# Performance work log

Measured on AMD Instinct MI355X. Metric: run time of the kernel, lower is better.

Reference implementation:

```python
import jax, jax.numpy as jnp
import numpy as np
from jax import lax

B, CIN, L = 2048, 1024, 30
E, C = 8, 2            # num_experts, num_classes
FC_IN = 256 * 9        # 2304
FIN_IN = C + 512 * L + 256 * (L // 2 + 1)  # 19458


def _maxpool1d(x):
    # MaxPool1d(kernel=2, stride=2, padding=1); pad with -inf like torch
    return lax.reduce_window(x, -jnp.inf, lax.max,
                             (1, 1, 2), (1, 1, 2),
                             [(0, 0), (0, 0), (1, 1)])


def _conv1d(x, w):
    # x: [B,Cin,L], w: [Cout,Cin,3], padding=1
    return lax.conv_general_dilated(x, w, (1,), [(1, 1)],
                                    dimension_numbers=('NCH', 'OIH', 'NCH'))


def setup_inputs() -> dict:
    key = jax.random.key(0)
    ks = jax.random.split(key, 16)
    s = 0.02
    inp = {
        'x': jax.random.normal(ks[0], (B, CIN, L), jnp.float32),
        'expert_idx': jax.random.randint(ks[1], (B,), 0, E),
        'conv1_w': jax.random.normal(ks[2], (512, 1024, 3), jnp.float32) * s,
        'conv1_b': jnp.zeros((512,), jnp.float32),
        'conv2_w': jax.random.normal(ks[3], (256, 512, 3), jnp.float32) * s,
        'conv2_b': jnp.zeros((256,), jnp.float32),
        'fc_w': jax.random.normal(ks[4], (1024, FC_IN), jnp.float32) * s,
        'fc_b': jnp.zeros((1024,), jnp.float32),
        'e_w1': jax.random.normal(ks[5], (E, 512, 1024), jnp.float32) * s,
        'e_b1': jnp.zeros((E, 512), jnp.float32),
        'e_w2': jax.random.normal(ks[6], (E, C, 512), jnp.float32) * s,
        'e_b2': jnp.zeros((E, C), jnp.float32),
        'agg_w': jax.random.normal(ks[7], (C, E * C), jnp.float32) * s,
        'agg_b': jnp.zeros((C,), jnp.float32),
        'fin_w': jax.random.normal(ks[8], (C, FIN_IN), jnp.float32) * s,
        'fin_b': jnp.zeros((C,), jnp.float32),
    }
    return inp


def reference(x, expert_idx, conv1_w, conv1_b, conv2_w, conv2_b, fc_w, fc_b,
              e_w1, e_b1, e_w2, e_b2, agg_w, agg_b, fin_w, fin_b):
    b = x.shape[0]
    # shared feature extractor
    x1 = jax.nn.relu(_conv1d(x, conv1_w) + conv1_b[None, :, None])     # [B,512,30]
    p1 = _maxpool1d(x1)                                                 # [B,512,16]
    x2 = jax.nn.relu(_conv1d(p1, conv2_w) + conv2_b[None, :, None])    # [B,256,16]
    p2 = _maxpool1d(x2)                                                 # [B,256,9]
    sf = jax.nn.relu(p2.reshape(b, -1) @ fc_w.T + fc_b)                 # [B,1024]

    # expert dispatch: run all experts densely, then select per-sample
    h = jax.nn.relu(jnp.einsum('bd,ehd->beh', sf, e_w1) + e_b1)        # [B,E,512]
    all_out = jnp.einsum('beh,ech->bec', h, e_w2) + e_b2               # [B,E,C]
    sel = all_out[jnp.arange(b), expert_idx]                           # [B,C]
    oh = jax.nn.one_hot(expert_idx, E, dtype=sel.dtype)                # [B,E]
    expert_outputs = (oh[:, :, None] * sel[:, None, :]).reshape(b, E * C)

    agg = expert_outputs @ agg_w.T + agg_b                             # [B,C]
    combined = jnp.concatenate(
        [agg, x1.reshape(b, -1), x2.reshape(b, -1)], axis=1)           # [B,19458]
    return combined @ fin_w.T + fin_b                                  # [B,C]
```

## Files before the change

kernel.cpp:

```cpp
#include <hip/hip_runtime.h>
#include <hip/hip_bf16.h>

typedef short short8 __attribute__((ext_vector_type(8)));
typedef short short4v __attribute__((ext_vector_type(4)));
typedef float f32x4 __attribute__((ext_vector_type(4)));

__device__ __forceinline__ float bf2f(short s) {
  return __builtin_bit_cast(float, (unsigned)((unsigned short)s) << 16);
}
__device__ __forceinline__ short f2bf(float f) {
  return __builtin_bit_cast(short, __float2bfloat16(f));
}
__device__ __forceinline__ void g2lds16(const void* g, void* l) {
  __builtin_amdgcn_global_load_lds((const __attribute__((address_space(1))) void*)g,
                                   (__attribute__((address_space(3))) void*)l, 16, 0, 0);
}


__global__ __launch_bounds__(256) void prep_x(const float* __restrict__ x, short* __restrict__ xt) {
  __shared__ float tile[64 * 30];
  const int b = blockIdx.x, ci0 = blockIdx.y * 64, t = threadIdx.x;
  const float* src = x + ((long)b * 1024 + ci0) * 30;
  for (int i = t; i < 1920; i += 256) tile[i] = src[i];
  __syncthreads();
  short* dst = xt + (long)b * 32 * 1024 + ci0;
  for (int i = t; i < 2048; i += 256) {
    int lp = i >> 6, ci = i & 63;
    float v = (lp == 0 || lp == 31) ? 0.f : tile[ci * 30 + lp - 1];
    dst[(long)lp * 1024 + ci] = f2bf(v);
  }
}

__global__ __launch_bounds__(256) void prep_weights(
    const float* __restrict__ conv1_w, const float* __restrict__ conv2_w,
    const float* __restrict__ fc_w, const float* __restrict__ e_w1,
    const float* __restrict__ fin_w,
    short* __restrict__ w1t, short* __restrict__ w2t, short* __restrict__ fcwt,
    short* __restrict__ ew1t, float* __restrict__ finw1, float* __restrict__ finw2) {
  const int T0 = 1572864;
  const int T1 = T0 + 393216;
  const int T2 = T1 + 2359296;
  const int T3 = T2 + 4194304;
  const int T4 = T3 + 30720;
  const int T5 = T4 + 8192;
  for (long idx = (long)blockIdx.x * 256 + threadIdx.x; idx < T5;
       idx += (long)gridDim.x * 256) {
    if (idx < T0) {
      int i = (int)idx; int co = i / 3072, j = i % 3072, k = j >> 10, ci = j & 1023;
      w1t[i] = f2bf(conv1_w[(co * 1024 + ci) * 3 + k]);
    } else if (idx < T1) {
      int i = (int)(idx - T0); int co = i / 1536, j = i % 1536, k = j >> 9, ci = j & 511;
      w2t[i] = f2bf(conv2_w[(co * 512 + ci) * 3 + k]);
    } else if (idx < T2) {
      int i = (int)(idx - T1); int n = i / 2304, j = i % 2304, jj = j >> 8, co = j & 255;
      fcwt[i] = f2bf(fc_w[n * 2304 + co * 9 + jj]);
    } else if (idx < T3) {
      int i = (int)(idx - T2);
      ew1t[i] = f2bf(e_w1[i]);
    } else if (idx < T4) {
      int i = (int)(idx - T3); int c = i / 15360, r = i % 15360, l = r >> 9, co = r & 511;
      finw1[i] = fin_w[c * 19458 + 2 + co * 30 + l];
    } else {
      int i = (int)(idx - T4); int c = i / 4096, r = i % 4096, l = r >> 8, co = r & 255;
      finw2[i] = fin_w[c * 19458 + 2 + 15360 + co * 16 + l];
    }
  }
}

__global__ __launch_bounds__(512, 2) void gemm256_bt_relu(
    const short* __restrict__ A, const short* __restrict__ Bm, short* __restrict__ C,
    const float* __restrict__ bias, int N, int K, int L, int S1, int S2, int nNB) {
  __shared__ __align__(16) short lA0[256 * 64], lA1[256 * 64];
  __shared__ __align__(16) short lB0[256 * 64], lB1[256 * 64];
  const int t = threadIdx.x, wave = t >> 6, lane = t & 63;
  const int wr = wave >> 2, wc = wave & 3;
  const int nwg = gridDim.x, qn = nwg >> 3, bid = blockIdx.x;
  const int swz = (bid & 7) * qn + (bid >> 3);
  const int m0 = (swz / nNB) * 256, n0 = (swz % nNB) * 256;
  const int srow = t >> 3;
  const int scol = ((t & 7) ^ (srow & 7)) * 8;

  long aoff[4], boff[4];
#pragma unroll
  for (int q = 0; q < 4; ++q) {
    int m = m0 + q * 64 + srow;
    aoff[q] = (long)(m / L) * S1 + (long)(m % L) * S2 + scol;
    boff[q] = (long)(n0 + q * 64 + srow) * K + scol;
  }
  const int ldst = wave * 512 + lane * 8;

  f32x4 acc[8][4];
#pragma unroll
  for (int i = 0; i < 8; ++i)
#pragma unroll
    for (int j = 0; j < 4; ++j) acc[i][j] = f32x4{0.f, 0.f, 0.f, 0.f};

  const int l7 = lane & 7, g4 = lane >> 4, r16 = lane & 15;
  const int nK = K >> 6;

#define STAGE256(k0, dA, dB) do {                                     \
    const long kk0_ = (long)(k0);                                     \
    _Pragma("unroll")                                                 \
    for (int q = 0; q < 4; ++q) {                                     \
      g2lds16(A + aoff[q] + kk0_, &dA[q * 4096 + ldst]);              \
      g2lds16(Bm + boff[q] + kk0_, &dB[q * 4096 + ldst]);             \
    } } while (0)

#define PHASES256(sA, sB) do {                                                        \
    short8 af[4][2], bfr[4][2];                                                       \
                                 \
    _Pragma("unroll") for (int kk = 0; kk < 2; ++kk) {                                \
      const int jb = ((kk * 4 + g4) ^ l7) * 8;                                        \
      _Pragma("unroll") for (int i = 0; i < 4; ++i)                                   \
        af[i][kk] = *(const short8*)&sA[(wr * 128 + i * 16 + r16) * 64 + jb];         \
      _Pragma("unroll") for (int j = 0; j < 2; ++j)                                   \
        bfr[j][kk] = *(const short8*)&sB[(wc * 64 + j * 16 + r16) * 64 + jb];         \
    }                                                                                 \
    __builtin_amdgcn_s_setprio(1);                                                    \
    _Pragma("unroll") for (int i = 0; i < 4; ++i)                                     \
    _Pragma("unroll") for (int j = 0; j < 2; ++j)                                     \
    _Pragma("unroll") for (int kk = 0; kk < 2; ++kk)                                  \
      acc[i][j] = __builtin_amdgcn_mfma_f32_16x16x32_bf16(af[i][kk], bfr[j][kk], acc[i][j], 0, 0, 0); \
    __builtin_amdgcn_s_setprio(0);                                                    \
                                         \
    _Pragma("unroll") for (int kk = 0; kk < 2; ++kk) {                                \
      const int jb = ((kk * 4 + g4) ^ l7) * 8;                                        \
      _Pragma("unroll") for (int j = 0; j < 2; ++j)                                   \
        bfr[2 + j][kk] = *(const short8*)&sB[(wc * 64 + (2 + j) * 16 + r16) * 64 + jb]; \
    }                                                                                 \
    __builtin_amdgcn_s_setprio(1);                                                    \
    _Pragma("unroll") for (int i = 0; i < 4; ++i)                                     \
    _Pragma("unroll") for (int j = 0; j < 2; ++j)                                     \
    _Pragma("unroll") for (int kk = 0; kk < 2; ++kk)                                  \
      acc[i][2 + j] = __builtin_amdgcn_mfma_f32_16x16x32_bf16(af[i][kk], bfr[2 + j][kk], acc[i][2 + j], 0, 0, 0); \
    __builtin_amdgcn_s_setprio(0);                                                    \
                                         \
    _Pragma("unroll") for (int kk = 0; kk < 2; ++kk) {                                \
      const int jb = ((kk * 4 + g4) ^ l7) * 8;                                        \
      _Pragma("unroll") for (int i = 0; i < 4; ++i)                                   \
        af[i][kk] = *(const short8*)&sA[(wr * 128 + (4 + i) * 16 + r16) * 64 + jb];   \
    }                                                                                 \
    __builtin_amdgcn_s_setprio(1);                                                    \
    _Pragma("unroll") for (int i = 0; i < 4; ++i)                                     \
    _Pragma("unroll") for (int j = 0; j < 2; ++j)                                     \
    _Pragma("unroll") for (int kk = 0; kk < 2; ++kk)                                  \
      acc[4 + i][2 + j] = __builtin_amdgcn_mfma_f32_16x16x32_bf16(af[i][kk], bfr[2 + j][kk], acc[4 + i][2 + j], 0, 0, 0); \
    __builtin_amdgcn_s_setprio(0);                                                    \
                                \
    __builtin_amdgcn_s_setprio(1);                                                    \
    _Pragma("unroll") for (int i = 0; i < 4; ++i)                                     \
    _Pragma("unroll") for (int j = 0; j < 2; ++j)                                     \
    _Pragma("unroll") for (int kk = 0; kk < 2; ++kk)                                  \
      acc[4 + i][j] = __builtin_amdgcn_mfma_f32_16x16x32_bf16(af[i][kk], bfr[j][kk], acc[4 + i][j], 0, 0, 0); \
    __builtin_amdgcn_s_setprio(0);                                                    \
  } while (0)

  STAGE256(0, lA0, lB0);
  for (int ktp = 0; ktp < (nK >> 1); ++ktp) {
    const int t1 = 2 * ktp + 1;
    __syncthreads();
    STAGE256((long)t1 << 6, lA1, lB1);
    PHASES256(lA0, lB0);
    __syncthreads();
    if (t1 + 1 < nK) STAGE256((long)(t1 + 1) << 6, lA0, lB0);
    PHASES256(lA1, lB1);
  }

#pragma unroll
  for (int j = 0; j < 4; ++j) {
    int col = n0 + wc * 64 + j * 16 + r16;
    float bv = bias[col];
#pragma unroll
    for (int i = 0; i < 8; ++i) {
      int rbase = m0 + wr * 128 + i * 16 + (g4 << 2);
#pragma unroll
      for (int r = 0; r < 4; ++r) {
        float o = fmaxf(acc[i][j][r] + bv, 0.f);
        C[(long)(rbase + r) * N + col] = f2bf(o);
      }
    }
  }
#undef STAGE256
#undef PHASES256
}

__global__ __launch_bounds__(256) void gemm_bt_relu(
    const short* __restrict__ A, const short* __restrict__ Bm, short* __restrict__ C,
    const float* __restrict__ bias, int N, int K, int L, int S1, int S2, int nNB) {
  __shared__ __align__(16) short lA[128 * 64];
  __shared__ __align__(16) short lB[128 * 64];
  const int t = threadIdx.x, wave = t >> 6, lane = t & 63;
  const int wr = wave >> 1, wc = wave & 1;
  const int nwg = gridDim.x, q = nwg >> 3, bid = blockIdx.x;
  const int swz = (bid & 7) * q + (bid >> 3);
  const int m0 = (swz / nNB) * 128, n0 = (swz % nNB) * 128;
  const int arow = t >> 3;
  const int sw8 = arow & 7;
  const int acolg = (((t & 7) ^ sw8) * 8);

  long aoff[4], boff[4];
#pragma unroll
  for (int qq = 0; qq < 4; ++qq) {
    int m = m0 + qq * 32 + arow;
    aoff[qq] = (long)(m / L) * S1 + (long)(m % L) * S2 + acolg;
    boff[qq] = (long)(n0 + qq * 32 + arow) * K + acolg;
  }

  f32x4 acc[4][4];
#pragma unroll
  for (int i = 0; i < 4; ++i)
#pragma unroll
    for (int j = 0; j < 4; ++j) acc[i][j] = f32x4{0.f, 0.f, 0.f, 0.f};

  const int l7 = lane & 7, g4 = lane >> 4, r16 = lane & 15;
  const int nK = K >> 6;
  for (int kt = 0; kt < nK; ++kt) {
    const int k0 = kt << 6;
#pragma unroll
    for (int qq = 0; qq < 4; ++qq) {
      g2lds16(A + aoff[qq] + k0, &lA[qq * 2048 + wave * 512 + lane * 8]);
      g2lds16(Bm + boff[qq] + k0, &lB[qq * 2048 + wave * 512 + lane * 8]);
    }
    __syncthreads();
#pragma unroll
    for (int kk = 0; kk < 2; ++kk) {
      const int jblk = ((kk * 4 + g4) ^ l7) * 8;
      short8 af[4], bfv[4];
#pragma unroll
      for (int i = 0; i < 4; ++i)
        af[i] = *(const short8*)&lA[(wr * 64 + i * 16 + r16) * 64 + jblk];
#pragma unroll
      for (int j = 0; j < 4; ++j)
        bfv[j] = *(const short8*)&lB[(wc * 64 + j * 16 + r16) * 64 + jblk];
#pragma unroll
      for (int i = 0; i < 4; ++i)
#pragma unroll
        for (int j = 0; j < 4; ++j)
          acc[i][j] = __builtin_amdgcn_mfma_f32_16x16x32_bf16(af[i], bfv[j], acc[i][j], 0, 0, 0);
    }
    __syncthreads();
  }

#pragma unroll
  for (int j = 0; j < 4; ++j) {
    int col = n0 + wc * 64 + j * 16 + (lane & 15);
    float bv = bias[col];
#pragma unroll
    for (int i = 0; i < 4; ++i) {
      int rbase = m0 + wr * 64 + i * 16 + ((lane >> 4) << 2);
#pragma unroll
      for (int r = 0; r < 4; ++r) {
        float o = fmaxf(acc[i][j][r] + bv, 0.f);
        C[(long)(rbase + r) * N + col] = f2bf(o);
      }
    }
  }
}

__global__ __launch_bounds__(256) void pool1(const short* __restrict__ x1t, short* __restrict__ p1t) {
  const long total = (long)2048 * 18 * 128;
  for (long idx = (long)blockIdx.x * 256 + threadIdx.x; idx < total;
       idx += (long)gridDim.x * 256) {
    int c4 = (int)(idx & 127); long tmp = idx >> 7; int jp = (int)(tmp % 18); long b = tmp / 18;
    short4v v = {0, 0, 0, 0};
    if (jp >= 1 && jp <= 16) {
      int j = jp - 1;
      int l0 = 2 * j - 1, l1 = 2 * j;
      short4v a = (l0 >= 0) ? *(const short4v*)&x1t[(b * 30 + l0) * 512 + c4 * 4] : short4v{0, 0, 0, 0};
      short4v bb = (l1 < 30) ? *(const short4v*)&x1t[(b * 30 + l1) * 512 + c4 * 4] : short4v{0, 0, 0, 0};
#pragma unroll
      for (int u = 0; u < 4; ++u) v[u] = f2bf(fmaxf(bf2f(a[u]), bf2f(bb[u])));
    }
    *(short4v*)&p1t[idx * 4] = v;
  }
}

__global__ __launch_bounds__(256) void pool2(const short* __restrict__ x2t, short* __restrict__ p2t) {
  const long total = (long)2048 * 9 * 64;
  for (long idx = (long)blockIdx.x * 256 + threadIdx.x; idx < total;
       idx += (long)gridDim.x * 256) {
    int c4 = (int)(idx & 63); long tmp = idx >> 6; int j = (int)(tmp % 9); long b = tmp / 9;
    int l0 = 2 * j - 1, l1 = 2 * j;
    short4v a = (l0 >= 0) ? *(const short4v*)&x2t[(b * 16 + l0) * 256 + c4 * 4] : short4v{0, 0, 0, 0};
    short4v bb = (l1 < 16) ? *(const short4v*)&x2t[(b * 16 + l1) * 256 + c4 * 4] : short4v{0, 0, 0, 0};
    short4v v;
#pragma unroll
    for (int u = 0; u < 4; ++u) v[u] = f2bf(fmaxf(bf2f(a[u]), bf2f(bb[u])));
    *(short4v*)&p2t[idx * 4] = v;
  }
}

__global__ __launch_bounds__(256) void final_k(
    const short* __restrict__ h, const short* __restrict__ x1t, const short* __restrict__ x2t,
    const int* __restrict__ eidx, const float* __restrict__ e_w2, const float* __restrict__ e_b2,
    const float* __restrict__ agg_w, const float* __restrict__ agg_b,
    const float* __restrict__ fin_w, const float* __restrict__ fin_b,
    const float* __restrict__ finw1, const float* __restrict__ finw2,
    float* __restrict__ out) {
  const int b = blockIdx.x, t = threadIdx.x, lane = t & 63, wave = t >> 6;
  const int e = eidx[b];
  float s0 = 0.f, s1 = 0.f, f0 = 0.f, f1 = 0.f;
  {
    const short* hp = h + (long)b * 4096 + e * 512;
    const float* w20 = e_w2 + (e * 2 + 0) * 512;
    const float* w21 = e_w2 + (e * 2 + 1) * 512;
    for (int i = t; i < 512; i += 256) {
      float hv = bf2f(hp[i]);
      s0 += hv * w20[i];
      s1 += hv * w21[i];
    }
  }
  {
    const short* xp = x1t + (long)b * 15360;
#pragma unroll
    for (int it = 0; it < 15; ++it) {
      int i = (it * 256 + t) * 4;
      short4v xv = *(const short4v*)&xp[i];
      float4 w0 = *(const float4*)&finw1[i];
      float4 w1 = *(const float4*)&finw1[15360 + i];
      float a0 = bf2f(xv[0]), a1 = bf2f(xv[1]), a2 = bf2f(xv[2]), a3 = bf2f(xv[3]);
      f0 += a0 * w0.x + a1 * w0.y + a2 * w0.z + a3 * w0.w;
      f1 += a0 * w1.x + a1 * w1.y + a2 * w1.z + a3 * w1.w;
    }
    const short* x2p = x2t + (long)b * 4096;
#pragma unroll
    for (int it = 0; it < 4; ++it) {
      int i = (it * 256 + t) * 4;
      short4v xv = *(const short4v*)&x2p[i];
      float4 w0 = *(const float4*)&finw2[i];
      float4 w1 = *(const float4*)&finw2[4096 + i];
      float a0 = bf2f(xv[0]), a1 = bf2f(xv[1]), a2 = bf2f(xv[2]), a3 = bf2f(xv[3]);
      f0 += a0 * w0.x + a1 * w0.y + a2 * w0.z + a3 * w0.w;
      f1 += a0 * w1.x + a1 * w1.y + a2 * w1.z + a3 * w1.w;
    }
  }
#pragma unroll
  for (int off = 32; off > 0; off >>= 1) {
    s0 += __shfl_down(s0, off);
    s1 += __shfl_down(s1, off);
    f0 += __shfl_down(f0, off);
    f1 += __shfl_down(f1, off);
  }
  __shared__ float red[4][4];
  if (lane == 0) { red[wave][0] = s0; red[wave][1] = s1; red[wave][2] = f0; red[wave][3] = f1; }
  __syncthreads();
  if (t == 0) {
    float S0 = 0, S1 = 0, F0 = 0, F1 = 0;
    for (int w = 0; w < 4; ++w) { S0 += red[w][0]; S1 += red[w][1]; F0 += red[w][2]; F1 += red[w][3]; }
    float sel0 = S0 + e_b2[e * 2 + 0];
    float sel1 = S1 + e_b2[e * 2 + 1];
    float agg0 = sel0 * agg_w[e * 2] + sel1 * agg_w[e * 2 + 1] + agg_b[0];
    float agg1 = sel0 * agg_w[16 + e * 2] + sel1 * agg_w[16 + e * 2 + 1] + agg_b[1];
    out[b * 2 + 0] = F0 + agg0 * fin_w[0] + agg1 * fin_w[1] + fin_b[0];
    out[b * 2 + 1] = F1 + agg0 * fin_w[19458 + 0] + agg1 * fin_w[19458 + 1] + fin_b[1];
  }
}

extern "C" void kernel_launch(void* const* d_in, const int* in_sizes, int n_in,
                              void* d_out, int out_size, void* d_ws, size_t ws_size,
                              hipStream_t stream) {
  const float* x       = (const float*)d_in[0];
  const int*   eidx    = (const int*)d_in[1];
  const float* conv1_w = (const float*)d_in[2];
  const float* conv1_b = (const float*)d_in[3];
  const float* conv2_w = (const float*)d_in[4];
  const float* conv2_b = (const float*)d_in[5];
  const float* fc_w    = (const float*)d_in[6];
  const float* fc_b    = (const float*)d_in[7];
  const float* e_w1    = (const float*)d_in[8];
  const float* e_b1    = (const float*)d_in[9];
  const float* e_w2    = (const float*)d_in[10];
  const float* e_b2    = (const float*)d_in[11];
  const float* agg_w   = (const float*)d_in[12];
  const float* agg_b   = (const float*)d_in[13];
  const float* fin_w   = (const float*)d_in[14];
  const float* fin_b   = (const float*)d_in[15];
  float* out = (float*)d_out;

  char* ws = (char*)d_ws;
  short* xt    = (short*)(ws + 0L);
  short* x1t   = (short*)(ws + 134217728L);
  short* p1t   = (short*)(ws + 197132288L);
  short* x2t   = (short*)(ws + 234881024L);
  short* p2t   = (short*)(ws + 251658240L);
  short* sf    = (short*)(ws + 261095424L);
  short* h     = (short*)(ws + 265289728L);
  short* w1t   = (short*)(ws + 282066944L);
  short* w2t   = (short*)(ws + 285212672L);
  short* fcwt  = (short*)(ws + 285999104L);
  short* ew1t  = (short*)(ws + 290717696L);
  float* finw1 = (float*)(ws + 299106304L);
  float* finw2 = (float*)(ws + 299229184L);

  prep_weights<<<4096, 256, 0, stream>>>(conv1_w, conv2_w, fc_w, e_w1, fin_w,
                                         w1t, w2t, fcwt, ew1t, finw1, finw2);
  prep_x<<<dim3(2048, 16), 256, 0, stream>>>(x, xt);
  gemm256_bt_relu<<<480, 512, 0, stream>>>(xt, w1t, x1t, conv1_b, 512, 3072, 30, 32768, 1024, 2);
  pool1<<<2048, 256, 0, stream>>>(x1t, p1t);
  gemm_bt_relu<<<512, 256, 0, stream>>>(p1t, w2t, x2t, conv2_b, 256, 1536, 16, 9216, 512, 2);
  pool2<<<1024, 256, 0, stream>>>(x2t, p2t);
  gemm_bt_relu<<<128, 256, 0, stream>>>(p2t, fcwt, sf, fc_b, 1024, 2304, 1, 2304, 0, 8);
  gemm_bt_relu<<<512, 256, 0, stream>>>(sf, ew1t, h, e_b1, 4096, 1024, 1, 1024, 0, 32);
  final_k<<<2048, 256, 0, stream>>>(h, x1t, x2t, eidx, e_w2, e_b2, agg_w, agg_b,
                                    fin_w, fin_b, finw1, finw2, out);
}
```

Before: 445.1 us.

## Double-buffer LDS in 128-tile GEMM and vectorize input transpose

Converts the 128x128 GEMM used for conv2, fc and expert layer 1 to double-buffered LDS. The next K tile is prefetched while MFMAs run on the current one, with s_setprio raised around the MFMA block. This removes one barrier-bound load stall per K step but doubles LDS use per block. The input transpose kernel also switches to float4 loads and 4-wide bf16 stores, cutting memory instruction count.

```diff
diff --git a/kernel.cpp b/kernel.cpp
--- a/kernel.cpp
+++ b/kernel.cpp
@@ -21,13 +21,18 @@
   __shared__ float tile[64 * 30];
   const int b = blockIdx.x, ci0 = blockIdx.y * 64, t = threadIdx.x;
   const float* src = x + ((long)b * 1024 + ci0) * 30;
-  for (int i = t; i < 1920; i += 256) tile[i] = src[i];
+  for (int i = t; i < 480; i += 256)
+    ((float4*)tile)[i] = ((const float4*)src)[i];
   __syncthreads();
   short* dst = xt + (long)b * 32 * 1024 + ci0;
-  for (int i = t; i < 2048; i += 256) {
-    int lp = i >> 6, ci = i & 63;
-    float v = (lp == 0 || lp == 31) ? 0.f : tile[ci * 30 + lp - 1];
-    dst[(long)lp * 1024 + ci] = f2bf(v);
+  for (int i = t; i < 512; i += 256) {
+    int lp = i >> 4, cq = i & 15;
+    short4v v = {0, 0, 0, 0};
+    if (lp >= 1 && lp <= 30) {
+#pragma unroll
+      for (int u = 0; u < 4; ++u) v[u] = f2bf(tile[(cq * 4 + u) * 30 + lp - 1]);
+    }
+    *(short4v*)&dst[(long)lp * 1024 + cq * 4] = v;
   }
 }
 
@@ -78,7 +83,7 @@
   const int swz = (bid & 7) * qn + (bid >> 3);
   const int m0 = (swz / nNB) * 256, n0 = (swz % nNB) * 256;
   const int srow = t >> 3;
-  const int scol = ((t & 7) ^ (srow & 7)) * 8;
+  const int scol = (((t & 7) ^ (srow & 7)) * 8);
 
   long aoff[4], boff[4];
 #pragma unroll
@@ -184,19 +189,18 @@
 #undef PHASES256
 }
 
-__global__ __launch_bounds__(256) void gemm_bt_relu(
+__global__ __launch_bounds__(256, 2) void gemm128_bt_relu(
     const short* __restrict__ A, const short* __restrict__ Bm, short* __restrict__ C,
     const float* __restrict__ bias, int N, int K, int L, int S1, int S2, int nNB) {
-  __shared__ __align__(16) short lA[128 * 64];
-  __shared__ __align__(16) short lB[128 * 64];
+  __shared__ __align__(16) short lA0[128 * 64], lA1[128 * 64];
+  __shared__ __align__(16) short lB0[128 * 64], lB1[128 * 64];
   const int t = threadIdx.x, wave = t >> 6, lane = t & 63;
   const int wr = wave >> 1, wc = wave & 1;
-  const int nwg = gridDim.x, q = nwg >> 3, bid = blockIdx.x;
-  const int swz = (bid & 7) * q + (bid >> 3);
+  const int nwg = gridDim.x, qn = nwg >> 3, bid = blockIdx.x;
+  const int swz = (bid & 7) * qn + (bid >> 3);
   const int m0 = (swz / nNB) * 128, n0 = (swz % nNB) * 128;
   const int arow = t >> 3;
-  const int sw8 = arow & 7;
-  const int acolg = (((t & 7) ^ sw8) * 8);
+  const int acolg = (((t & 7) ^ (arow & 7)) * 8);
 
   long aoff[4], boff[4];
 #pragma unroll
@@ -205,6 +209,7 @@
     aoff[qq] = (long)(m / L) * S1 + (long)(m % L) * S2 + acolg;
     boff[qq] = (long)(n0 + qq * 32 + arow) * K + acolg;
   }
+  const int ldst = wave * 512 + lane * 8;
 
   f32x4 acc[4][4];
 #pragma unroll
@@ -214,40 +219,49 @@
 
   const int l7 = lane & 7, g4 = lane >> 4, r16 = lane & 15;
   const int nK = K >> 6;
-  for (int kt = 0; kt < nK; ++kt) {
-    const int k0 = kt << 6;
-#pragma unroll
-    for (int qq = 0; qq < 4; ++qq) {
-      g2lds16(A + aoff[qq] + k0, &lA[qq * 2048 + wave * 512 + lane * 8]);
-      g2lds16(Bm + boff[qq] + k0, &lB[qq * 2048 + wave * 512 + lane * 8]);
-    }
+
+#define STAGE128(k0, dA, dB) do {                                     \
+    const long kk0_ = (long)(k0);                                     \
+    _Pragma("unroll")                                                 \
+    for (int qq = 0; qq < 4; ++qq) {                                  \
+      g2lds16(A + aoff[qq] + kk0_, &dA[qq * 2048 + ldst]);            \
+      g2lds16(Bm + boff[qq] + kk0_, &dB[qq * 2048 + ldst]);           \
+    } } while (0)
+
+#define PHASES128(sA, sB) do {                                                        \
+    _Pragma("unroll")                                                                 \
+    for (int kk = 0; kk < 2; ++kk) {                                                  \
+      const int jblk = ((kk * 4 + g4) ^ l7) * 8;                                      \
+      short8 af[4], bfv[4];                                                           \
+      _Pragma("unroll") for (int i = 0; i < 4; ++i)                                   \
+        af[i] = *(const short8*)&sA[(wr * 64 + i * 16 + r16) * 64 + jblk];            \
+      _Pragma("unroll") for (int j = 0; j < 4; ++j)                                   \
+        bfv[j] = *(const short8*)&sB[(wc * 64 + j * 16 + r16) * 64 + jblk];           \
+      __builtin_amdgcn_s_setprio(1);                                                  \
+      _Pragma("unroll") for (int i = 0; i < 4; ++i)                                   \
+      _Pragma("unroll") for (int j = 0; j < 4; ++j)                                   \
+        acc[i][j] = __builtin_amdgcn_mfma_f32_16x16x32_bf16(af[i], bfv[j], acc[i][j], 0, 0, 0); \
+      __builtin_amdgcn_s_setprio(0);                                                  \
+    } } while (0)
+
+  STAGE128(0, lA0, lB0);
+  for (int ktp = 0; ktp < (nK >> 1); ++ktp) {
+    const int t1 = 2 * ktp + 1;
     __syncthreads();
-#pragma unroll
-    for (int kk = 0; kk < 2; ++kk) {
-      const int jblk = ((kk * 4 + g4) ^ l7) * 8;
-      short8 af[4], bfv[4];
-#pragma unroll
-      for (int i = 0; i < 4; ++i)
-        af[i] = *(const short8*)&lA[(wr * 64 + i * 16 + r16) * 64 + jblk];
-#pragma unroll
-      for (int j = 0; j < 4; ++j)
-        bfv[j] = *(const short8*)&lB[(wc * 64 + j * 16 + r16) * 64 + jblk];
-#pragma unroll
-      for (int i = 0; i < 4; ++i)
-#pragma unroll
-        for (int j = 0; j < 4; ++j)
-          acc[i][j] = __builtin_amdgcn_mfma_f32_16x16x32_bf16(af[i], bfv[j], acc[i][j], 0, 0, 0);
-    }
+    STAGE128((long)t1 << 6, lA1, lB1);
+    PHASES128(lA0, lB0);
     __syncthreads();
+    if (t1 + 1 < nK) STAGE128((long)(t1 + 1) << 6, lA0, lB0);
+    PHASES128(lA1, lB1);
   }
 
 #pragma unroll
   for (int j = 0; j < 4; ++j) {
-    int col = n0 + wc * 64 + j * 16 + (lane & 15);
+    int col = n0 + wc * 64 + j * 16 + r16;
     float bv = bias[col];
 #pragma unroll
     for (int i = 0; i < 4; ++i) {
-      int rbase = m0 + wr * 64 + i * 16 + ((lane >> 4) << 2);
+      int rbase = m0 + wr * 64 + i * 16 + (g4 << 2);
 #pragma unroll
       for (int r = 0; r < 4; ++r) {
         float o = fmaxf(acc[i][j][r] + bv, 0.f);
@@ -255,6 +269,8 @@
       }
     }
   }
+#undef STAGE128
+#undef PHASES128
 }
 
 __global__ __launch_bounds__(256) void pool1(const short* __restrict__ x1t, short* __restrict__ p1t) {
@@ -397,10 +413,10 @@
   prep_x<<<dim3(2048, 16), 256, 0, stream>>>(x, xt);
   gemm256_bt_relu<<<480, 512, 0, stream>>>(xt, w1t, x1t, conv1_b, 512, 3072, 30, 32768, 1024, 2);
   pool1<<<2048, 256, 0, stream>>>(x1t, p1t);
-  gemm_bt_relu<<<512, 256, 0, stream>>>(p1t, w2t, x2t, conv2_b, 256, 1536, 16, 9216, 512, 2);
+  gemm128_bt_relu<<<512, 256, 0, stream>>>(p1t, w2t, x2t, conv2_b, 256, 1536, 16, 9216, 512, 2);
   pool2<<<1024, 256, 0, stream>>>(x2t, p2t);
-  gemm_bt_relu<<<128, 256, 0, stream>>>(p2t, fcwt, sf, fc_b, 1024, 2304, 1, 2304, 0, 8);
-  gemm_bt_relu<<<512, 256, 0, stream>>>(sf, ew1t, h, e_b1, 4096, 1024, 1, 1024, 0, 32);
+  gemm128_bt_relu<<<128, 256, 0, stream>>>(p2t, fcwt, sf, fc_b, 1024, 2304, 1, 2304, 0, 8);
+  gemm128_bt_relu<<<512, 256, 0, stream>>>(sf, ew1t, h, e_b1, 4096, 1024, 1, 1024, 0, 32);
   final_k<<<2048, 256, 0, stream>>>(h, x1t, x2t, eidx, e_w2, e_b2, agg_w, agg_b,
                                     fin_w, fin_b, finw1, finw2, out);
 }
```

Result: faster. 398.0 us (-10.6%).
